# Kernel tuning notes

Hardware: AMD Instinct MI355X
Metric: run time of the kernel (lower is better)

## Reference

```python
import jax, jax.numpy as jnp
import numpy as np

D_MODEL = 512
NUM_NEURONS = 4
D_STATE = 16
D_CONV = 4
EXPAND = 2
D_INNER = EXPAND * D_MODEL  # 1024
DT_RANK = -(-D_MODEL // 16)  # ceil -> 32
B_SZ, L_SEQ = 2, 1024


def setup_inputs() -> dict:
    key = jax.random.key(0)
    ks = jax.random.split(key, 8)
    C = NUM_NEURONS * D_INNER
    return {
        "x": jax.random.normal(ks[0], (B_SZ, NUM_NEURONS, L_SEQ, D_MODEL), jnp.float32),
        "in_proj_w": jax.random.normal(ks[1], (2 * D_INNER, D_MODEL), jnp.float32) * 0.02,
        "conv_w": jax.random.normal(ks[2], (C, 1, D_CONV), jnp.float32) * 0.1,
        "conv_b": jax.random.normal(ks[3], (C,), jnp.float32) * 0.01,
        "x_proj_w": jax.random.normal(ks[4], (DT_RANK + 2 * D_STATE, D_INNER), jnp.float32) * 0.02,
        "dt_proj_w": jax.random.normal(ks[5], (D_INNER, DT_RANK), jnp.float32) * 0.02,
        "dt_proj_b": jax.random.normal(ks[6], (D_INNER,), jnp.float32) * 0.01,
        "A_log": jnp.log(jnp.tile(jnp.arange(1, D_STATE + 1, dtype=jnp.float32), (D_INNER, 1))),
        "D_param": jnp.ones((D_INNER,), jnp.float32),
        "out_proj_w": jax.random.normal(ks[7], (D_MODEL, D_INNER), jnp.float32) * 0.02,
    }


def _ssm(x_flat, dt, A, Bs, Cs, D_param):
    # x_flat: [BN, L, di]; dt: [BN, L, di]; A: [di, ds]; Bs/Cs: [BN, L, ds]
    dt = jnp.minimum(dt, 2.5)

    def step(h, inp):
        x_t, dt_t, B_t, C_t = inp            # [BN,di], [BN,di], [BN,ds], [BN,ds]
        dA = jnp.exp(dt_t[:, :, None] * A)   # [BN, di, ds]
        dB = dt_t[:, :, None] * B_t[:, None, :]
        h = dA * h + dB * x_t[:, :, None]
        y_t = jnp.einsum('bds,bs->bd', h, C_t)
        return h, y_t

    h0 = jnp.zeros((x_flat.shape[0], D_INNER, D_STATE), x_flat.dtype)
    xs = (jnp.swapaxes(x_flat, 0, 1), jnp.swapaxes(dt, 0, 1),
          jnp.swapaxes(Bs, 0, 1), jnp.swapaxes(Cs, 0, 1))
    _, ys = jax.lax.scan(step, h0, xs)       # ys: [L, BN, di]
    return jnp.swapaxes(ys, 0, 1) + x_flat * D_param


def reference(x, in_proj_w, conv_w, conv_b, x_proj_w, dt_proj_w, dt_proj_b,
              A_log, D_param, out_proj_w):
    B, N, L, _ = x.shape
    silu = jax.nn.silu
    x_and_res = jnp.einsum('bnld,ed->bnle', x, in_proj_w)
    x_in, res = x_and_res[..., :D_INNER], x_and_res[..., D_INNER:]
    # depthwise causal conv over L, channels = N*d_inner
    xc = jnp.transpose(x_in, (0, 1, 3, 2)).reshape(B, N * D_INNER, L)
    xc = jax.lax.conv_general_dilated(
        xc, conv_w, window_strides=(1,), padding=[(D_CONV - 1, 0)],
        dimension_numbers=('NCH', 'OIH', 'NCH'),
        feature_group_count=N * D_INNER) + conv_b[None, :, None]
    x_conv = silu(jnp.transpose(xc.reshape(B, N, D_INNER, L), (0, 1, 3, 2)))
    x_flat = x_conv.reshape(B * N, L, D_INNER)
    proj = jnp.einsum('bli,pi->blp', x_flat, x_proj_w)
    dt_r = proj[..., :DT_RANK]
    Bs = proj[..., DT_RANK:DT_RANK + D_STATE]
    Cs = proj[..., DT_RANK + D_STATE:]
    dt = jax.nn.softplus(jnp.einsum('blr,dr->bld', dt_r, dt_proj_w) + dt_proj_b)
    A = -jnp.exp(A_log)
    y = _ssm(x_flat, dt, A, Bs, Cs, D_param)
    y = y.reshape(B, N, L, D_INNER)
    return jnp.einsum('bnli,oi->bnlo', y * silu(res), out_proj_w)
```

## Files before the change

kernel.cpp:

```cpp
#include <hip/hip_runtime.h>
#include <cstdint>
#include <cstddef>

#define DMODEL 512
#define DINNER 1024
#define DSTATE 16
#define DTRANK 32
#define LSEQ   1024
#define NSEQ   8
#define NTOK   8192
#define NC     32
#define CL     32

typedef unsigned short ushort_t;
typedef __bf16 bf16x8 __attribute__((ext_vector_type(8)));
typedef float  f32x4  __attribute__((ext_vector_type(4)));
typedef unsigned short u16x8 __attribute__((ext_vector_type(8)));
typedef unsigned short u16x4 __attribute__((ext_vector_type(4)));

__device__ __forceinline__ ushort_t f2b(float f) {
    unsigned int u = __float_as_uint(f);
    u += 0x7fffu + ((u >> 16) & 1u);
    return (ushort_t)(u >> 16);
}

__device__ __forceinline__ void gload_lds16(const void* g, void* l) {
    __builtin_amdgcn_global_load_lds(
        (__attribute__((address_space(1))) void*)(void*)g,
        (__attribute__((address_space(3))) void*)l, 16, 0, 0);
}

__device__ __forceinline__ void pow_chain16(float E, float* dec) {
    const float E2 = E * E, E4 = E2 * E2, E8 = E4 * E4;
    dec[0] = E;        dec[1] = E2;       dec[2] = E2 * E;   dec[3] = E4;
    dec[4] = E4 * E;   dec[5] = E4 * E2;  dec[6] = E4 * dec[2]; dec[7] = E8;
    dec[8] = E8 * E;   dec[9] = E8 * E2;  dec[10] = E8 * dec[2]; dec[11] = E8 * E4;
    dec[12] = E8 * dec[4]; dec[13] = E8 * dec[5]; dec[14] = E8 * dec[6]; dec[15] = E8 * E8;
}

template<int BM, int BN, int WR, int WC, int WTM, int WTN>
__global__ __launch_bounds__(256)
void gemm_mfma(const ushort_t* __restrict__ A, const ushort_t* __restrict__ W,
               float* __restrict__ C, int K, int lda, int ldw, int ldc)
{
    static_assert(WR * WC == 4 && WR * WTM * 16 == BM && WC * WTN * 16 == BN, "tile");
    __shared__ __align__(16) ushort_t Al[BM * 32];
    __shared__ __align__(16) ushort_t Wl[BN * 32];
    const int tid  = threadIdx.x;
    const int wave = tid >> 6, lane = tid & 63;
    const int wr = wave / WC, wc = wave % WC;
    const int q = lane >> 4, r16 = lane & 15;
    const int m0 = blockIdx.y * BM, n0 = blockIdx.x * BN;

    f32x4 acc[WTM][WTN] = {};

    for (int kk = 0; kk < K; kk += 32) {
#pragma unroll
        for (int it = 0; it < BM * 4 / 256; ++it) {
            const int i = it * 256 + tid;
            const int r = i >> 2, c = i & 3;
            gload_lds16(&A[(size_t)(m0 + r) * lda + kk + c * 8], &Al[i * 8]);
        }
#pragma unroll
        for (int it = 0; it < BN * 4 / 256; ++it) {
            const int i = it * 256 + tid;
            const int r = i >> 2, c = i & 3;
            gload_lds16(&W[(size_t)(n0 + r) * ldw + kk + c * 8], &Wl[i * 8]);
        }
        __syncthreads();

        bf16x8 af[WTM], bfr[WTN];
#pragma unroll
        for (int i = 0; i < WTM; ++i)
            af[i] = *(const bf16x8*)&Al[(wr * WTM * 16 + i * 16 + r16) * 32 + q * 8];
#pragma unroll
        for (int j = 0; j < WTN; ++j)
            bfr[j] = *(const bf16x8*)&Wl[(wc * WTN * 16 + j * 16 + r16) * 32 + q * 8];
#pragma unroll
        for (int i = 0; i < WTM; ++i)
#pragma unroll
            for (int j = 0; j < WTN; ++j)
                acc[i][j] = __builtin_amdgcn_mfma_f32_16x16x32_bf16(af[i], bfr[j], acc[i][j], 0, 0, 0);
        __syncthreads();
    }

#pragma unroll
    for (int i = 0; i < WTM; ++i) {
#pragma unroll
        for (int j = 0; j < WTN; ++j) {
            const int n = n0 + wc * WTN * 16 + j * 16 + r16;
#pragma unroll
            for (int t = 0; t < 4; ++t) {
                const int m = m0 + wr * WTM * 16 + i * 16 + q * 4 + t;
                C[(size_t)m * ldc + n] = acc[i][j][t];
            }
        }
    }
}

__global__ __launch_bounds__(256)
void cvt_all4(const float* __restrict__ x,   const float* __restrict__ inw,
              const float* __restrict__ xpw, const float* __restrict__ outw,
              ushort_t* __restrict__ xb,   ushort_t* __restrict__ inwb,
              ushort_t* __restrict__ xpwb, ushort_t* __restrict__ outwb)
{
    const int g = (blockIdx.x * 256 + threadIdx.x) * 4;
    const float* src; ushort_t* dst; int off;
    if (g < 4194304)      { src = x;    dst = xb;    off = g; }
    else if (g < 5242880) { src = inw;  dst = inwb;  off = g - 4194304; }
    else if (g < 5308416) { src = xpw;  dst = xpwb;  off = g - 5242880; }
    else                  { src = outw; dst = outwb; off = g - 5308416; }
    const f32x4 v = *(const f32x4*)&src[off];
    u16x4 o; o[0] = f2b(v[0]); o[1] = f2b(v[1]); o[2] = f2b(v[2]); o[3] = f2b(v[3]);
    *(u16x4*)&dst[off] = o;
}

__global__ __launch_bounds__(256)
void conv_silu(const float* __restrict__ xr, const float* __restrict__ cw,
               const float* __restrict__ cb, float* __restrict__ xc,
               ushort_t* __restrict__ xcb)
{
    const int idx = blockIdx.x * 256 + threadIdx.x;
    const int i = idx & (DINNER - 1);
    const int t = idx >> 10;
    const int l = t & (LSEQ - 1);
    const int n = (t >> 10) & 3;
    const int c = n * DINNER + i;
    float acc = cb[c];
    const float w0 = cw[c * 4 + 0], w1 = cw[c * 4 + 1];
    const float w2 = cw[c * 4 + 2], w3 = cw[c * 4 + 3];
    const size_t rowb = (size_t)t * (2 * DINNER) + i;
    if (l >= 3) acc += xr[rowb - 3 * 2048] * w0;
    if (l >= 2) acc += xr[rowb - 2 * 2048] * w1;
    if (l >= 1) acc += xr[rowb - 1 * 2048] * w2;
    acc += xr[rowb] * w3;
    const float v = acc / (1.f + __expf(-acc));
    xc[idx]  = v;
    xcb[idx] = f2b(v);
}

__global__ __launch_bounds__(256)
void ssm_phase1(const float* __restrict__ xc,
                const float* __restrict__ proj,
                const float* __restrict__ dtw, const float* __restrict__ dtb,
                float* __restrict__ hend, float* __restrict__ dts)
{
    __shared__ __align__(16) float Lp[CL * 64];
    const int tid  = threadIdx.x;
    const int c    = blockIdx.x & (NC - 1);
    const int dgrp = (blockIdx.x >> 5) & 3;
    const int seq  = blockIdx.x >> 7;
    const int d    = dgrp * 256 + tid;
    const int t0   = seq * LSEQ + c * CL;

#pragma unroll
    for (int it = 0; it < 8; ++it)
        Lp[it * 256 + tid] = proj[(size_t)t0 * 64 + it * 256 + tid];

    float w[DTRANK];
#pragma unroll
    for (int r4 = 0; r4 < DTRANK; r4 += 4) {
        const f32x4 v = *(const f32x4*)&dtw[d * DTRANK + r4];
        w[r4] = v[0]; w[r4 + 1] = v[1]; w[r4 + 2] = v[2]; w[r4 + 3] = v[3];
    }
    const float bias = dtb[d];
    __syncthreads();

    float h[DSTATE] = {};
    float dtsum = 0.f;
#pragma unroll 2
    for (int l = 0; l < CL; ++l) {
        const float xv = xc[(size_t)(t0 + l) * 1024 + d];
        const float* lp = &Lp[l * 64];
        float v = bias;
#pragma unroll
        for (int r4 = 0; r4 < DTRANK; r4 += 4) {
            const f32x4 p = *(const f32x4*)&lp[r4];
            v = fmaf(p[0], w[r4 + 0], v); v = fmaf(p[1], w[r4 + 1], v);
            v = fmaf(p[2], w[r4 + 2], v); v = fmaf(p[3], w[r4 + 3], v);
        }
        const float dt = fminf(__logf(1.f + __expf(v)), 2.5f);
        dtsum += dt;
        const float dtx = dt * xv;
        float dec[DSTATE];
        pow_chain16(__expf(-dt), dec);
#pragma unroll
        for (int s4 = 0; s4 < DSTATE; s4 += 4) {
            const f32x4 Bv = *(const f32x4*)&lp[DTRANK + s4];
#pragma unroll
            for (int u = 0; u < 4; ++u)
                h[s4 + u] = fmaf(dec[s4 + u], h[s4 + u], Bv[u] * dtx);
        }
    }

    const size_t base = ((size_t)((seq * NC + c) * 1024 + d)) * DSTATE;
#pragma unroll
    for (int s4 = 0; s4 < DSTATE; s4 += 4)
        *(f32x4*)&hend[base + s4] = f32x4{h[s4], h[s4 + 1], h[s4 + 2], h[s4 + 3]};
    dts[(seq * NC + c) * 1024 + d] = dtsum;
}

__global__ __launch_bounds__(256)
void ssm_phase2(float* __restrict__ hend,
                const float* __restrict__ dts,
                const float* __restrict__ A_log)
{
    const int gid = blockIdx.x * 256 + threadIdx.x;
    const int s   = gid & 15;
    const int d   = (gid >> 4) & 1023;
    const int seq = gid >> 14;
    const float Av = -__expf(A_log[d * DSTATE + s]);
    float h = 0.f;
#pragma unroll 4
    for (int c = 0; c < NC; ++c) {
        const size_t idx = ((size_t)((seq * NC + c) * 1024 + d)) * DSTATE + s;
        const float he = hend[idx];
        const float P  = __expf(Av * dts[(seq * NC + c) * 1024 + d]);
        hend[idx] = h;
        h = P * h + he;
    }
}

__global__ __launch_bounds__(256)
void ssm_phase3(const float* __restrict__ xr,
                const float* __restrict__ xc,
                const float* __restrict__ proj,
                const float* __restrict__ dtw, const float* __restrict__ dtb,
                const float* __restrict__ Dp,
                const float* __restrict__ hin,
                ushort_t* __restrict__ zb)
{
    __shared__ __align__(16) float Lp[CL * 64];
    const int tid  = threadIdx.x;
    const int c    = blockIdx.x & (NC - 1);
    const int dgrp = (blockIdx.x >> 5) & 3;
    const int seq  = blockIdx.x >> 7;
    const int d    = dgrp * 256 + tid;
    const int t0   = seq * LSEQ + c * CL;

#pragma unroll
    for (int it = 0; it < 8; ++it)
        Lp[it * 256 + tid] = proj[(size_t)t0 * 64 + it * 256 + tid];

    float w[DTRANK];
#pragma unroll
    for (int r4 = 0; r4 < DTRANK; r4 += 4) {
        const f32x4 v = *(const f32x4*)&dtw[d * DTRANK + r4];
        w[r4] = v[0]; w[r4 + 1] = v[1]; w[r4 + 2] = v[2]; w[r4 + 3] = v[3];
    }
    const float bias = dtb[d];
    const float Dv = Dp[d];

    float h[DSTATE];
    const size_t base = ((size_t)((seq * NC + c) * 1024 + d)) * DSTATE;
#pragma unroll
    for (int s4 = 0; s4 < DSTATE; s4 += 4) {
        const f32x4 v = *(const f32x4*)&hin[base + s4];
        h[s4] = v[0]; h[s4 + 1] = v[1]; h[s4 + 2] = v[2]; h[s4 + 3] = v[3];
    }
    __syncthreads();

#pragma unroll 2
    for (int l = 0; l < CL; ++l) {
        const int t = t0 + l;
        const float xv = xc[(size_t)t * 1024 + d];
        const float* lp = &Lp[l * 64];
        float v = bias;
#pragma unroll
        for (int r4 = 0; r4 < DTRANK; r4 += 4) {
            const f32x4 p = *(const f32x4*)&lp[r4];
            v = fmaf(p[0], w[r4 + 0], v); v = fmaf(p[1], w[r4 + 1], v);
            v = fmaf(p[2], w[r4 + 2], v); v = fmaf(p[3], w[r4 + 3], v);
        }
        const float dt = fminf(__logf(1.f + __expf(v)), 2.5f);
        const float dtx = dt * xv;
        float dec[DSTATE];
        pow_chain16(__expf(-dt), dec);
        float y = 0.f;
#pragma unroll
        for (int s4 = 0; s4 < DSTATE; s4 += 4) {
            const f32x4 Bv = *(const f32x4*)&lp[DTRANK + s4];
            const f32x4 Cv = *(const f32x4*)&lp[DTRANK + DSTATE + s4];
#pragma unroll
            for (int u = 0; u < 4; ++u) {
                h[s4 + u] = fmaf(dec[s4 + u], h[s4 + u], Bv[u] * dtx);
                y = fmaf(h[s4 + u], Cv[u], y);
            }
        }
        const float r = xr[(size_t)t * 2048 + DINNER + d];
        const float z = (y + xv * Dv) * (r / (1.f + __expf(-r)));
        zb[(size_t)t * 1024 + d] = f2b(z);
    }
}

extern "C" void kernel_launch(void* const* d_in, const int* in_sizes, int n_in,
                              void* d_out, int out_size, void* d_ws, size_t ws_size,
                              hipStream_t stream)
{
    const float* x        = (const float*)d_in[0];
    const float* in_w     = (const float*)d_in[1];
    const float* conv_w   = (const float*)d_in[2];
    const float* conv_b   = (const float*)d_in[3];
    const float* xproj_w  = (const float*)d_in[4];
    const float* dtproj_w = (const float*)d_in[5];
    const float* dtproj_b = (const float*)d_in[6];
    const float* A_log    = (const float*)d_in[7];
    const float* D_param  = (const float*)d_in[8];
    const float* out_w    = (const float*)d_in[9];
    float* out = (float*)d_out;

    char* ws = (char*)d_ws;
    float*    xr    = (float*)ws;
    float*    xc    = (float*)(ws + (size_t)NTOK * 2048 * 4);
    ushort_t* xb    = (ushort_t*)(ws + (size_t)NTOK * 2048 * 4);
    float*    proj  = (float*)(ws + (size_t)NTOK * 3072 * 4);
    ushort_t* xcb   = (ushort_t*)(ws + (size_t)NTOK * 3072 * 4 + (size_t)NTOK * 64 * 4);
    ushort_t* zb    = xcb;
    ushort_t* inwb  = (ushort_t*)(ws + (size_t)NTOK * 3072 * 4 + (size_t)NTOK * 64 * 4 + (size_t)NTOK * 1024 * 2);
    ushort_t* xpwb  = inwb + 2048 * 512;
    ushort_t* outwb = xpwb + 64 * 1024;
    float*    hend  = (float*)(ws + 118u * 1024 * 1024);
    float*    dts   = hend + (size_t)NSEQ * NC * 1024 * DSTATE;

    cvt_all4<<<5696, 256, 0, stream>>>(x, in_w, xproj_w, out_w, xb, inwb, xpwb, outwb);
    gemm_mfma<128, 128, 2, 2, 4, 4><<<dim3(16, 64), 256, 0, stream>>>(xb, inwb, xr, 512, 512, 512, 2048);
    conv_silu<<<NTOK * DINNER / 256, 256, 0, stream>>>(xr, conv_w, conv_b, xc, xcb);
    gemm_mfma<64, 64, 2, 2, 2, 2><<<dim3(1, 128), 256, 0, stream>>>(xcb, xpwb, proj, 1024, 1024, 1024, 64);
    ssm_phase1<<<NSEQ * 4 * NC, 256, 0, stream>>>(xc, proj, dtproj_w, dtproj_b, hend, dts);
    ssm_phase2<<<NSEQ * 1024 * DSTATE / 256, 256, 0, stream>>>(hend, dts, A_log);
    ssm_phase3<<<NSEQ * 4 * NC, 256, 0, stream>>>(xr, xc, proj, dtproj_w, dtproj_b, D_param, hend, zb);
    gemm_mfma<64, 128, 1, 4, 4, 2><<<dim3(4, 128), 256, 0, stream>>>(zb, outwb, out, 1024, 1024, 1024, 512);
}
```

Before: 254.7 us.

## Fuse silu of residual into in_proj epilogue and use bf16 intermediates

The in_proj GEMM epilogue now writes the x half in fp32 compactly and applies silu to the residual half, storing it as bf16. The conv kernel drops its fp32 output, and both SSM phases read the bf16 conv output and the bf16 silu residual instead of fp32 buffers. This cuts global memory traffic between stages, at the cost of bf16 rounding of x and of the gate in the scan.

```diff
diff --git a/kernel.cpp b/kernel.cpp
--- a/kernel.cpp
+++ b/kernel.cpp
@@ -23,6 +23,9 @@
     u += 0x7fffu + ((u >> 16) & 1u);
     return (ushort_t)(u >> 16);
 }
+__device__ __forceinline__ float b2f(ushort_t u) {
+    return __uint_as_float(((unsigned)u) << 16);
+}
 
 __device__ __forceinline__ void gload_lds16(const void* g, void* l) {
     __builtin_amdgcn_global_load_lds(
@@ -38,10 +41,11 @@
     dec[12] = E8 * dec[4]; dec[13] = E8 * dec[5]; dec[14] = E8 * dec[6]; dec[15] = E8 * E8;
 }
 
-template<int BM, int BN, int WR, int WC, int WTM, int WTN>
+template<int BM, int BN, int WR, int WC, int WTM, int WTN, int EPI>
 __global__ __launch_bounds__(256)
 void gemm_mfma(const ushort_t* __restrict__ A, const ushort_t* __restrict__ W,
-               float* __restrict__ C, int K, int lda, int ldw, int ldc)
+               float* __restrict__ C, ushort_t* __restrict__ Cb,
+               int K, int lda, int ldw, int ldc)
 {
     static_assert(WR * WC == 4 && WR * WTM * 16 == BM && WC * WTN * 16 == BN, "tile");
     __shared__ __align__(16) ushort_t Al[BM * 32];
@@ -92,7 +96,17 @@
 #pragma unroll
             for (int t = 0; t < 4; ++t) {
                 const int m = m0 + wr * WTM * 16 + i * 16 + q * 4 + t;
-                C[(size_t)m * ldc + n] = acc[i][j][t];
+                const float v = acc[i][j][t];
+                if (EPI == 0) {
+                    C[(size_t)m * ldc + n] = v;
+                } else {
+                    if (n < DINNER) {
+                        C[(size_t)m * DINNER + n] = v;
+                    } else {
+                        const float sv = v / (1.f + __expf(-v));
+                        Cb[(size_t)m * DINNER + (n - DINNER)] = f2b(sv);
+                    }
+                }
             }
         }
     }
@@ -116,9 +130,8 @@
 }
 
 __global__ __launch_bounds__(256)
-void conv_silu(const float* __restrict__ xr, const float* __restrict__ cw,
-               const float* __restrict__ cb, float* __restrict__ xc,
-               ushort_t* __restrict__ xcb)
+void conv_silu(const float* __restrict__ xi, const float* __restrict__ cw,
+               const float* __restrict__ cb, ushort_t* __restrict__ xcb)
 {
     const int idx = blockIdx.x * 256 + threadIdx.x;
     const int i = idx & (DINNER - 1);
@@ -129,18 +142,17 @@
     float acc = cb[c];
     const float w0 = cw[c * 4 + 0], w1 = cw[c * 4 + 1];
     const float w2 = cw[c * 4 + 2], w3 = cw[c * 4 + 3];
-    const size_t rowb = (size_t)t * (2 * DINNER) + i;
-    if (l >= 3) acc += xr[rowb - 3 * 2048] * w0;
-    if (l >= 2) acc += xr[rowb - 2 * 2048] * w1;
-    if (l >= 1) acc += xr[rowb - 1 * 2048] * w2;
-    acc += xr[rowb] * w3;
+    const size_t rowb = (size_t)t * DINNER + i;
+    if (l >= 3) acc += xi[rowb - 3 * DINNER] * w0;
+    if (l >= 2) acc += xi[rowb - 2 * DINNER] * w1;
+    if (l >= 1) acc += xi[rowb - 1 * DINNER] * w2;
+    acc += xi[rowb] * w3;
     const float v = acc / (1.f + __expf(-acc));
-    xc[idx]  = v;
     xcb[idx] = f2b(v);
 }
 
 __global__ __launch_bounds__(256)
-void ssm_phase1(const float* __restrict__ xc,
+void ssm_phase1(const ushort_t* __restrict__ xcb,
                 const float* __restrict__ proj,
                 const float* __restrict__ dtw, const float* __restrict__ dtb,
                 float* __restrict__ hend, float* __restrict__ dts)
@@ -170,7 +182,7 @@
     float dtsum = 0.f;
 #pragma unroll 2
     for (int l = 0; l < CL; ++l) {
-        const float xv = xc[(size_t)(t0 + l) * 1024 + d];
+        const float xv = b2f(xcb[(size_t)(t0 + l) * 1024 + d]);
         const float* lp = &Lp[l * 64];
         float v = bias;
 #pragma unroll
@@ -222,8 +234,8 @@
 }
 
 __global__ __launch_bounds__(256)
-void ssm_phase3(const float* __restrict__ xr,
-                const float* __restrict__ xc,
+void ssm_phase3(const ushort_t* __restrict__ rsb,
+                const ushort_t* __restrict__ xcb,
                 const float* __restrict__ proj,
                 const float* __restrict__ dtw, const float* __restrict__ dtb,
                 const float* __restrict__ Dp,
@@ -263,7 +275,7 @@
 #pragma unroll 2
     for (int l = 0; l < CL; ++l) {
         const int t = t0 + l;
-        const float xv = xc[(size_t)t * 1024 + d];
+        const float xv = b2f(xcb[(size_t)t * 1024 + d]);
         const float* lp = &Lp[l * 64];
         float v = bias;
 #pragma unroll
@@ -287,8 +299,8 @@
                 y = fmaf(h[s4 + u], Cv[u], y);
             }
         }
-        const float r = xr[(size_t)t * 2048 + DINNER + d];
-        const float z = (y + xv * Dv) * (r / (1.f + __expf(-r)));
+        const float sr = b2f(rsb[(size_t)t * 1024 + d]);
+        const float z = (y + xv * Dv) * sr;
         zb[(size_t)t * 1024 + d] = f2b(z);
     }
 }
@@ -310,24 +322,24 @@
     float* out = (float*)d_out;
 
     char* ws = (char*)d_ws;
-    float*    xr    = (float*)ws;
-    float*    xc    = (float*)(ws + (size_t)NTOK * 2048 * 4);
-    ushort_t* xb    = (ushort_t*)(ws + (size_t)NTOK * 2048 * 4);
-    float*    proj  = (float*)(ws + (size_t)NTOK * 3072 * 4);
-    ushort_t* xcb   = (ushort_t*)(ws + (size_t)NTOK * 3072 * 4 + (size_t)NTOK * 64 * 4);
+    float*    xi    = (float*)ws;
+    ushort_t* rsb   = (ushort_t*)(ws + 32u * 1024 * 1024);
+    ushort_t* xcb   = (ushort_t*)(ws + 48u * 1024 * 1024);
     ushort_t* zb    = xcb;
-    ushort_t* inwb  = (ushort_t*)(ws + (size_t)NTOK * 3072 * 4 + (size_t)NTOK * 64 * 4 + (size_t)NTOK * 1024 * 2);
+    float*    proj  = (float*)(ws + 64u * 1024 * 1024);
+    ushort_t* xb    = (ushort_t*)(ws + 66u * 1024 * 1024);
+    ushort_t* inwb  = (ushort_t*)(ws + 74u * 1024 * 1024);
     ushort_t* xpwb  = inwb + 2048 * 512;
     ushort_t* outwb = xpwb + 64 * 1024;
-    float*    hend  = (float*)(ws + 118u * 1024 * 1024);
-    float*    dts   = hend + (size_t)NSEQ * NC * 1024 * DSTATE;
+    float*    hend  = (float*)(ws + 80u * 1024 * 1024);
+    float*    dts   = (float*)(ws + 96u * 1024 * 1024);
 
     cvt_all4<<<5696, 256, 0, stream>>>(x, in_w, xproj_w, out_w, xb, inwb, xpwb, outwb);
-    gemm_mfma<128, 128, 2, 2, 4, 4><<<dim3(16, 64), 256, 0, stream>>>(xb, inwb, xr, 512, 512, 512, 2048);
-    conv_silu<<<NTOK * DINNER / 256, 256, 0, stream>>>(xr, conv_w, conv_b, xc, xcb);
-    gemm_mfma<64, 64, 2, 2, 2, 2><<<dim3(1, 128), 256, 0, stream>>>(xcb, xpwb, proj, 1024, 1024, 1024, 64);
-    ssm_phase1<<<NSEQ * 4 * NC, 256, 0, stream>>>(xc, proj, dtproj_w, dtproj_b, hend, dts);
+    gemm_mfma<128, 128, 2, 2, 4, 4, 1><<<dim3(16, 64), 256, 0, stream>>>(xb, inwb, xi, rsb, 512, 512, 512, 0);
+    conv_silu<<<NTOK * DINNER / 256, 256, 0, stream>>>(xi, conv_w, conv_b, xcb);
+    gemm_mfma<64, 64, 2, 2, 2, 2, 0><<<dim3(1, 128), 256, 0, stream>>>(xcb, xpwb, proj, nullptr, 1024, 1024, 1024, 64);
+    ssm_phase1<<<NSEQ * 4 * NC, 256, 0, stream>>>(xcb, proj, dtproj_w, dtproj_b, hend, dts);
     ssm_phase2<<<NSEQ * 1024 * DSTATE / 256, 256, 0, stream>>>(hend, dts, A_log);
-    ssm_phase3<<<NSEQ * 4 * NC, 256, 0, stream>>>(xr, xc, proj, dtproj_w, dtproj_b, D_param, hend, zb);
-    gemm_mfma<64, 128, 1, 4, 4, 2><<<dim3(4, 128), 256, 0, stream>>>(zb, outwb, out, 1024, 1024, 1024, 512);
-}
+    ssm_phase3<<<NSEQ * 4 * NC, 256, 0, stream>>>(rsb, xcb, proj, dtproj_w, dtproj_b, D_param, hend, zb);
+    gemm_mfma<64, 128, 1, 4, 4, 2, 0><<<dim3(4, 128), 256, 0, stream>>>(zb, outwb, out, nullptr, 1024, 1024, 1024, 512);
+}
```

New measurement: 256.7 us. About the same (+0.8%).
